# Performance work log

Measured on AMD Instinct MI355X. Metric: run time of the kernel, lower is better.

The kernel has to match this reference:

```python
import jax, jax.numpy as jnp
import numpy as np

EMB = 1024
HEADS = 16
HEAD_SZ = EMB // HEADS
EPS = 1e-5


def _layernorm(x, g, b):
    mu = jnp.mean(x, axis=-1, keepdims=True)
    var = jnp.mean(jnp.square(x - mu), axis=-1, keepdims=True)
    return (x - mu) * jax.lax.rsqrt(var + EPS) * g + b


def setup_inputs() -> dict:
    key = jax.random.key(0)
    ks = jax.random.split(key, 12)
    s_in = 1.0 / np.sqrt(EMB)
    s_h = 1.0 / np.sqrt(4 * EMB)
    return {
        "x": jax.random.normal(ks[0], (4, 1024, EMB), jnp.float32),
        # per-head Q/K/V projections stacked: [H, EMB, HEAD_SZ], no bias
        "wq": jax.random.normal(ks[1], (HEADS, EMB, HEAD_SZ), jnp.float32) * s_in,
        "wk": jax.random.normal(ks[2], (HEADS, EMB, HEAD_SZ), jnp.float32) * s_in,
        "wv": jax.random.normal(ks[3], (HEADS, EMB, HEAD_SZ), jnp.float32) * s_in,
        "w_proj": jax.random.normal(ks[4], (EMB, EMB), jnp.float32) * s_in,
        "b_proj": jnp.zeros((EMB,), jnp.float32),
        "w1": jax.random.normal(ks[5], (EMB, 4 * EMB), jnp.float32) * s_in,
        "b1": jnp.zeros((4 * EMB,), jnp.float32),
        "w2": jax.random.normal(ks[6], (4 * EMB, EMB), jnp.float32) * s_h,
        "b2": jnp.zeros((EMB,), jnp.float32),
        "g1": jnp.ones((EMB,), jnp.float32),
        "be1": jnp.zeros((EMB,), jnp.float32),
        "g2": jnp.ones((EMB,), jnp.float32),
        "be2": jnp.zeros((EMB,), jnp.float32),
    }


def reference(x, wq, wk, wv, w_proj, b_proj, w1, b1, w2, b2, g1, be1, g2, be2):
    B, T, C = x.shape
    # --- self-attention (pre-norm) ---
    h = _layernorm(x, g1, be1)
    q = jnp.einsum("btc,hcd->bhtd", h, wq)
    k = jnp.einsum("btc,hcd->bhtd", h, wk)
    v = jnp.einsum("btc,hcd->bhtd", h, wv)
    scale = 1.0 / jnp.sqrt(jnp.asarray(HEAD_SZ, x.dtype))
    scores = jnp.einsum("bhtd,bhsd->bhts", q, k) * scale  # non-causal: SDPA called with no mask
    attn = jax.nn.softmax(scores, axis=-1)
    o = jnp.einsum("bhts,bhsd->bhtd", attn, v)
    o = o.transpose(0, 2, 1, 3).reshape(B, T, C)  # concat heads (same order as torch.cat)
    sa_out = o @ w_proj + b_proj
    x = x + sa_out
    # --- feed-forward; note ln2 applied twice, faithful to source ---
    t = _layernorm(x, g2, be2)
    t = _layernorm(t, g2, be2)
    ff = jax.nn.relu(t @ w1 + b1) @ w2 + b2
    return x + ff
```

## Files before the change

### kernel.cpp

```cpp
#include <hip/hip_runtime.h>
#include <hip/hip_bf16.h>
#include <math.h>
#include <stdint.h>

typedef __bf16 bf16_t;
typedef __bf16 bf16x4 __attribute__((ext_vector_type(4)));
typedef __bf16 bf16x8 __attribute__((ext_vector_type(8)));
typedef float floatx4 __attribute__((ext_vector_type(4)));

#define BM 128
#define BK 32

__device__ __forceinline__ size_t ftaddr(int m, int k, int KT) {
    return ((size_t)(m >> 4) * KT + (k >> 5)) * 512
         + (((k >> 3) & 3) * 16 + (m & 15)) * 8 + (k & 7);
}

__device__ __forceinline__ void gload16(const void* g, void* lds) {
    __builtin_amdgcn_global_load_lds(
        (__attribute__((address_space(1))) void*)(uintptr_t)g,
        (__attribute__((address_space(3))) void*)(uintptr_t)lds,
        16, 0, 0);
}

template<int N>
__device__ __forceinline__ void waitvm_barrier() {
    if constexpr (N == 0)       asm volatile("s_waitcnt vmcnt(0)\n\ts_barrier" ::: "memory");
    else if constexpr (N == 3)  asm volatile("s_waitcnt vmcnt(3)\n\ts_barrier" ::: "memory");
    else if constexpr (N == 4)  asm volatile("s_waitcnt vmcnt(4)\n\ts_barrier" ::: "memory");
    else if constexpr (N == 6)  asm volatile("s_waitcnt vmcnt(6)\n\ts_barrier" ::: "memory");
    else if constexpr (N == 8)  asm volatile("s_waitcnt vmcnt(8)\n\ts_barrier" ::: "memory");
    else if constexpr (N == 9)  asm volatile("s_waitcnt vmcnt(9)\n\ts_barrier" ::: "memory");
    else if constexpr (N == 12) asm volatile("s_waitcnt vmcnt(12)\n\ts_barrier" ::: "memory");
    else if constexpr (N == 16) asm volatile("s_waitcnt vmcnt(16)\n\ts_barrier" ::: "memory");
    else static_assert(N == 0, "unsupported vmcnt");
}

__device__ __forceinline__ void waitvm_barrier_rt(int n) {
    switch (n) {
    case 12: asm volatile("s_waitcnt vmcnt(12)\n\ts_barrier" ::: "memory"); break;
    case 9:  asm volatile("s_waitcnt vmcnt(9)\n\ts_barrier"  ::: "memory"); break;
    case 8:  asm volatile("s_waitcnt vmcnt(8)\n\ts_barrier"  ::: "memory"); break;
    case 6:  asm volatile("s_waitcnt vmcnt(6)\n\ts_barrier"  ::: "memory"); break;
    case 4:  asm volatile("s_waitcnt vmcnt(4)\n\ts_barrier"  ::: "memory"); break;
    case 3:  asm volatile("s_waitcnt vmcnt(3)\n\ts_barrier"  ::: "memory"); break;
    default: asm volatile("s_waitcnt vmcnt(0)\n\ts_barrier"  ::: "memory"); break;
    }
}

__global__ void prep_kernel(const float* __restrict__ wq, const float* __restrict__ wk,
                            const float* __restrict__ wv, const float* __restrict__ w_proj,
                            const float* __restrict__ w1, const float* __restrict__ w2,
                            bf16_t* __restrict__ WQKVT, bf16_t* __restrict__ WPROJT,
                            bf16_t* __restrict__ W1T, bf16_t* __restrict__ W2T,
                            const float* __restrict__ x, const float* __restrict__ g1,
                            const float* __restrict__ be1, bf16_t* __restrict__ HB)
{
    __shared__ __align__(16) char psm[33024];
    const int tid = threadIdx.x;
    if (blockIdx.x < 3072) {
        float (*tile)[65] = (float(*)[65])psm;
        const int idx = blockIdx.x;
        const float* in; bf16_t* out; int R, C, rt, ct; long nrow0;
        if (idx < 768) {
            const int z = idx >> 8;
            const int hd = (idx >> 4) & 15;
            rt = idx & 15; ct = 0; R = 1024; C = 64;
            in  = (z == 0 ? wq : z == 1 ? wk : wv) + hd * 65536;
            out = WQKVT; nrow0 = z * 1024 + hd * 64;
        } else if (idx < 1024) {
            const int t = idx - 768; rt = t & 15; ct = t >> 4; R = 1024; C = 1024;
            in = w_proj; out = WPROJT; nrow0 = 0;
        } else if (idx < 2048) {
            const int t = idx - 1024; rt = t & 15; ct = t >> 4; R = 1024; C = 4096;
            in = w1; out = W1T; nrow0 = 0;
        } else {
            const int t = idx - 2048; rt = t & 63; ct = t >> 6; R = 4096; C = 1024;
            in = w2; out = W2T; nrow0 = 0;
        }
        const int r0 = rt * 64, c0 = ct * 64;
        const int tr = tid >> 4;
        const int tc = (tid & 15) * 4;
#pragma unroll
        for (int rr = 0; rr < 4; rr++) {
            const int r = tr + rr * 16;
            const float4 v = *(const float4*)&in[(long)(r0 + r) * C + c0 + tc];
            tile[r][tc + 0] = v.x; tile[r][tc + 1] = v.y;
            tile[r][tc + 2] = v.z; tile[r][tc + 3] = v.w;
        }
        __syncthreads();
        const int KT = R >> 5;
        const int w = tid >> 6, l = tid & 63;
        const int c = l >> 4, rr2 = l & 15;
#pragma unroll
        for (int it = 0; it < 2; ++it) {
            const int t8 = it * 4 + w;
            const int kt = t8 >> 2;
            const int nb = t8 & 3;
            const long n = nrow0 + c0 + nb * 16 + rr2;
            const int k = r0 + kt * 32 + c * 8;
            bf16x8 o;
#pragma unroll
            for (int e = 0; e < 8; e++)
                o[e] = (bf16_t)tile[kt * 32 + c * 8 + e][nb * 16 + rr2];
            *(bf16x8*)&out[ftaddr((int)n, k, KT)] = o;
        }
    } else {
        bf16_t (*ybuf)[1032] = (bf16_t(*)[1032])psm;
        const int wave = tid >> 6, lane = tid & 63;
        const int rb = blockIdx.x - 3072;
        float4 gvv[4], bvv[4];
#pragma unroll
        for (int j = 0; j < 4; j++) {
            gvv[j] = ((const float4*)g1)[lane + j * 64];
            bvv[j] = ((const float4*)be1)[lane + j * 64];
        }
#pragma unroll
        for (int rr = 0; rr < 4; ++rr) {
            const int lrow = wave * 4 + rr;
            const float* xr = x + (size_t)(rb * 16 + lrow) * 1024;
            float4 v[4];
            float s = 0.f, s2 = 0.f;
#pragma unroll
            for (int j = 0; j < 4; j++) {
                v[j] = ((const float4*)xr)[lane + j * 64];
                s  += v[j].x + v[j].y + v[j].z + v[j].w;
                s2 += v[j].x * v[j].x + v[j].y * v[j].y + v[j].z * v[j].z + v[j].w * v[j].w;
            }
#pragma unroll
            for (int off = 32; off >= 1; off >>= 1) {
                s  += __shfl_xor(s, off);
                s2 += __shfl_xor(s2, off);
            }
            const float mu = s * (1.0f / 1024.0f);
            const float rs = rsqrtf(fmaxf(s2 * (1.0f / 1024.0f) - mu * mu, 0.f) + 1e-5f);
#pragma unroll
            for (int j = 0; j < 4; j++) {
                bf16x4 o;
                o[0] = (bf16_t)((v[j].x - mu) * rs * gvv[j].x + bvv[j].x);
                o[1] = (bf16_t)((v[j].y - mu) * rs * gvv[j].y + bvv[j].y);
                o[2] = (bf16_t)((v[j].z - mu) * rs * gvv[j].z + bvv[j].z);
                o[3] = (bf16_t)((v[j].w - mu) * rs * gvv[j].w + bvv[j].w);
                *(bf16x4*)&ybuf[lrow][(lane + j * 64) * 4] = o;
            }
        }
        __syncthreads();
        bf16_t* outBase = HB + (size_t)rb * 32 * 512;
#pragma unroll
        for (int it = 0; it < 8; ++it) {
            const int s = it * 256 + tid;
            const int kt = s >> 6, c = (s >> 4) & 3, rr2 = s & 15;
            const bf16x8 val = *(const bf16x8*)&ybuf[rr2][kt * 32 + c * 8];
            *(bf16x8*)&outBase[(size_t)s * 8] = val;
        }
    }
}

__global__ void ln2x_kernel(const float* __restrict__ x, const float* __restrict__ g,
                            const float* __restrict__ b, bf16_t* __restrict__ outb)
{
    __shared__ __align__(16) bf16_t ybuf[16][1032];
    const int tid = threadIdx.x, wave = tid >> 6, lane = tid & 63;
    const int rb = blockIdx.x;
    float4 gvv[4], bvv[4];
#pragma unroll
    for (int j = 0; j < 4; j++) {
        gvv[j] = ((const float4*)g)[lane + j * 64];
        bvv[j] = ((const float4*)b)[lane + j * 64];
    }
#pragma unroll
    for (int rr = 0; rr < 4; ++rr) {
        const int lrow = wave * 4 + rr;
        const float* xr = x + (size_t)(rb * 16 + lrow) * 1024;
        float4 v[4];
        float s = 0.f, s2 = 0.f;
#pragma unroll
        for (int j = 0; j < 4; j++) {
            v[j] = ((const float4*)xr)[lane + j * 64];
            s  += v[j].x + v[j].y + v[j].z + v[j].w;
            s2 += v[j].x * v[j].x + v[j].y * v[j].y + v[j].z * v[j].z + v[j].w * v[j].w;
        }
#pragma unroll
        for (int off = 32; off >= 1; off >>= 1) {
            s  += __shfl_xor(s, off);
            s2 += __shfl_xor(s2, off);
        }
        float mu = s * (1.0f / 1024.0f);
        float rs = rsqrtf(fmaxf(s2 * (1.0f / 1024.0f) - mu * mu, 0.f) + 1e-5f);
        s = 0.f; s2 = 0.f;
#pragma unroll
        for (int j = 0; j < 4; j++) {
            v[j].x = (v[j].x - mu) * rs * gvv[j].x + bvv[j].x;
            v[j].y = (v[j].y - mu) * rs * gvv[j].y + bvv[j].y;
            v[j].z = (v[j].z - mu) * rs * gvv[j].z + bvv[j].z;
            v[j].w = (v[j].w - mu) * rs * gvv[j].w + bvv[j].w;
            s  += v[j].x + v[j].y + v[j].z + v[j].w;
            s2 += v[j].x * v[j].x + v[j].y * v[j].y + v[j].z * v[j].z + v[j].w * v[j].w;
        }
#pragma unroll
        for (int off = 32; off >= 1; off >>= 1) {
            s  += __shfl_xor(s, off);
            s2 += __shfl_xor(s2, off);
        }
        mu = s * (1.0f / 1024.0f);
        rs = rsqrtf(fmaxf(s2 * (1.0f / 1024.0f) - mu * mu, 0.f) + 1e-5f);
#pragma unroll
        for (int j = 0; j < 4; j++) {
            bf16x4 o;
            o[0] = (bf16_t)((v[j].x - mu) * rs * gvv[j].x + bvv[j].x);
            o[1] = (bf16_t)((v[j].y - mu) * rs * gvv[j].y + bvv[j].y);
            o[2] = (bf16_t)((v[j].z - mu) * rs * gvv[j].z + bvv[j].z);
            o[3] = (bf16_t)((v[j].w - mu) * rs * gvv[j].w + bvv[j].w);
            *(bf16x4*)&ybuf[lrow][(lane + j * 64) * 4] = o;
        }
    }
    __syncthreads();
    bf16_t* outBase = outb + (size_t)rb * 32 * 512;
#pragma unroll
    for (int it = 0; it < 8; ++it) {
        const int s = it * 256 + tid;
        const int kt = s >> 6, c = (s >> 4) & 3, rr2 = s & 15;
        const bf16x8 val = *(const bf16x8*)&ybuf[rr2][kt * 32 + c * 8];
        *(bf16x8*)&outBase[(size_t)s * 8] = val;
    }
}

template<int EPI, int BNt, int DEPTH>
__global__ __launch_bounds__(256, 2)
void gemm_bt(const bf16_t* __restrict__ A, const bf16_t* __restrict__ Bt,
             const int K,
             const float* __restrict__ bias, const float* __restrict__ resid,
             float* __restrict__ outf, bf16_t* __restrict__ outb,
             bf16_t* __restrict__ aux1, bf16_t* __restrict__ aux2,
             const int Nout)
{
    constexpr int NFRAG = BNt / 16;
    constexpr int LPS = (BNt == 128) ? 4 : 3;
    constexpr int ASZ = DEPTH * 8 * 512;
    constexpr int BSZ = DEPTH * NFRAG * 512;
    __shared__ __align__(16) bf16_t smem[ASZ + BSZ];
    bf16_t* Asb = smem;
    bf16_t* Bsb = smem + ASZ;
    const int tid  = threadIdx.x;
    const int wave = tid >> 6, lane = tid & 63;
    const int bm = blockIdx.x * BM, bn = blockIdx.y * BNt;
    const int KT = K >> 5;

    floatx4 acc[2][NFRAG];
#pragma unroll
    for (int i = 0; i < 2; i++)
#pragma unroll
        for (int j = 0; j < NFRAG; j++) acc[i][j] = (floatx4){0.f, 0.f, 0.f, 0.f};

    const bf16_t* gA0 = A + ((size_t)(bm / 16 + wave * 2 + 0) * KT) * 512 + lane * 8;
    const bf16_t* gA1 = A + ((size_t)(bm / 16 + wave * 2 + 1) * KT) * 512 + lane * 8;
    const int lA0 = (wave * 2 + 0) * 512;
    const int lA1 = (wave * 2 + 1) * 512;

    const bf16_t* gB0;
    const bf16_t* gB1 = nullptr;
    int lB0, lB1 = 0;
    if (BNt == 128) {
        gB0 = Bt + ((size_t)(bn / 16 + wave * 2 + 0) * KT) * 512 + lane * 8;
        gB1 = Bt + ((size_t)(bn / 16 + wave * 2 + 1) * KT) * 512 + lane * 8;
        lB0 = (wave * 2 + 0) * 512;
        lB1 = (wave * 2 + 1) * 512;
    } else {
        gB0 = Bt + ((size_t)(bn / 16 + wave) * KT) * 512 + lane * 8;
        lB0 = wave * 512;
    }

    auto stage = [&](int t, int bu) {
        const size_t off = (size_t)t * 512;
        gload16(gA0 + off, Asb + bu * 4096 + lA0);
        gload16(gA1 + off, Asb + bu * 4096 + lA1);
        gload16(gB0 + off, Bsb + bu * (NFRAG * 512) + lB0);
        if (BNt == 128) gload16(gB1 + off, Bsb + bu * (NFRAG * 512) + lB1);
    };

    auto compute = [&](int bu) {
        bf16x8 af[2], bfv[NFRAG];
#pragma unroll
        for (int i = 0; i < 2; i++)
            af[i] = *(const bf16x8*)&Asb[bu * 4096 + (wave * 2 + i) * 512 + lane * 8];
#pragma unroll
        for (int j = 0; j < NFRAG; j++)
            bfv[j] = *(const bf16x8*)&Bsb[bu * (NFRAG * 512) + j * 512 + lane * 8];
#pragma unroll
        for (int i = 0; i < 2; i++)
#pragma unroll
            for (int j = 0; j < NFRAG; j++)
                acc[i][j] = __builtin_amdgcn_mfma_f32_16x16x32_bf16(af[i], bfv[j], acc[i][j], 0, 0, 0);
    };

    const int NT = K / BK;
#pragma unroll
    for (int i = 0; i < DEPTH - 1; ++i) stage(i, i);
    int bu = 0;
    for (int t = 0; t <= NT - DEPTH; ++t) {
        waitvm_barrier<LPS * (DEPTH - 2)>();
        stage(t + DEPTH - 1, bu == 0 ? DEPTH - 1 : bu - 1);
        compute(bu);
        bu = (bu + 1 == DEPTH) ? 0 : bu + 1;
    }
#pragma unroll
    for (int j = DEPTH - 2; j >= 0; --j) {
        waitvm_barrier_rt(LPS * j);
        compute(bu);
        bu = (bu + 1 == DEPTH) ? 0 : bu + 1;
    }

    const int er = (lane >> 4) * 4, ec = lane & 15;
    if (EPI == 0 && bn >= 2048) {
        __syncthreads();
        bf16_t* scr = smem;
#pragma unroll
        for (int i = 0; i < 2; i++)
#pragma unroll
            for (int j = 0; j < NFRAG; j++)
#pragma unroll
                for (int r = 0; r < 4; r++)
                    scr[(j * 16 + ec) * 136 + wave * 32 + i * 16 + er + r] =
                        (bf16_t)acc[i][j][r];
        __syncthreads();
        const int bq = bm >> 10, tmod = bm & 1023, h0 = (bn - 2048) >> 6;
#pragma unroll
        for (int it = 0; it < 8; ++it) {
            const int c = it * 256 + tid;
            const int dl = c >> 4, t16 = c & 15;
            const bf16x8 val = *(const bf16x8*)&scr[dl * 136 + t16 * 8];
            const int h = h0 + (dl >> 6), dd = dl & 63;
            *(bf16x8*)&aux2[(size_t)((bq * 16 + h) * 64 + dd) * 1024 + tmod + t16 * 8] = val;
        }
        return;
    }
#pragma unroll
    for (int i = 0; i < 2; i++) {
#pragma unroll
        for (int j = 0; j < NFRAG; j++) {
            const int col = bn + j * 16 + ec;
#pragma unroll
            for (int r = 0; r < 4; r++) {
                const int row = bm + wave * 32 + i * 16 + er + r;
                const float v = acc[i][j][r];
                if (EPI == 0) {
                    const int b = row >> 10, t = row & 1023;
                    if (col < 1024) {
                        const int h = col >> 6, d = col & 63;
                        outb[(size_t)((b * 16 + h) * 1024 + t) * 64 + d] = (bf16_t)v;
                    } else {
                        const int c2 = col - 1024, h = c2 >> 6, d = c2 & 63;
                        aux1[(size_t)((b * 16 + h) * 1024 + t) * 64 + d] = (bf16_t)v;
                    }
                } else if (EPI == 1 || EPI == 3) {
                    const size_t idx = (size_t)row * Nout + col;
                    outf[idx] = v + bias[col] + resid[idx];
                } else if (EPI == 2) {
                    outb[ftaddr(row, col, Nout >> 5)] = (bf16_t)fmaxf(v + bias[col], 0.f);
                }
            }
        }
    }
}

__global__ __launch_bounds__(256, 4)
void attn_kernel(const bf16_t* __restrict__ Q, const bf16_t* __restrict__ Kg,
                 const bf16_t* __restrict__ Vt, bf16_t* __restrict__ Og)
{
    __shared__ __align__(16) bf16_t Ks[2][4096];
    __shared__ __align__(16) bf16_t Vs[2][4096];
    __shared__ __align__(16) bf16_t Ps[4][1024];
    const int tid = threadIdx.x, wave = tid >> 6, lane = tid & 63;
    const int bh = blockIdx.y;
    const int b = bh >> 4, h = bh & 15;
    const int q0 = blockIdx.x * 64 + wave * 16;
    const bf16_t* Qb = Q + (size_t)bh * 65536;
    const char* Kb = (const char*)(Kg + (size_t)bh * 65536);
    const char* Vb = (const char*)(Vt + (size_t)bh * 65536);
    const int fr = lane & 15, g = lane >> 4, fk = g * 8;

    const bf16x8 qf0 = *(const bf16x8*)&Qb[(size_t)(q0 + fr) * 64 + fk];
    const bf16x8 qf1 = *(const bf16x8*)&Qb[(size_t)(q0 + fr) * 64 + 32 + fk];

    floatx4 o[4];
#pragma unroll
    for (int dt = 0; dt < 4; dt++) o[dt] = (floatx4){0.f, 0.f, 0.f, 0.f};
    float lsum[4] = {0.f, 0.f, 0.f, 0.f};
    bf16_t* pw = &Ps[wave][0];
    const float sscale = 0.125f * 1.44269504088896f;

    auto stage = [&](int s0, int bu) {
#pragma unroll
        for (int t = 0; t < 2; t++) {
            const int j = wave * 2 + t;
            gload16(Kb + (size_t)(s0 + lane) * 128 + j * 16, &Ks[bu][j * 512]);
            gload16(Vb + (size_t)lane * 2048 + (size_t)s0 * 2 + j * 16, &Vs[bu][j * 512]);
        }
    };

    stage(0, 0);
    int bu = 0;
    for (int it = 0; it < 16; ++it) {
        __syncthreads();
        if (it < 15) stage((it + 1) * 64, bu ^ 1);
        const bf16_t* Kl = Ks[bu];
        const bf16_t* Vl = Vs[bu];

        floatx4 sacc[4];
#pragma unroll
        for (int ss = 0; ss < 4; ss++) sacc[ss] = (floatx4){0.f, 0.f, 0.f, 0.f};
#pragma unroll
        for (int c = 0; c < 2; c++) {
            const int ch = c * 4 + g;
            const bf16x8 qf = (c == 0) ? qf0 : qf1;
#pragma unroll
            for (int ss = 0; ss < 4; ss++) {
                const bf16x8 kf = *(const bf16x8*)&Kl[ch * 512 + (ss * 16 + fr) * 8];
                sacc[ss] = __builtin_amdgcn_mfma_f32_16x16x32_bf16(qf, kf, sacc[ss], 0, 0, 0);
            }
        }
#pragma unroll
        for (int ss = 0; ss < 4; ss++) {
#pragma unroll
            for (int r = 0; r < 4; r++) {
                const float p = __builtin_amdgcn_exp2f(sacc[ss][r] * sscale);
                lsum[r] += p;
                const int q = g * 4 + r;
                pw[(ss * 2 + (fr >> 3)) * 128 + q * 8 + (fr & 7)] = (bf16_t)p;
            }
        }
        asm volatile("s_waitcnt lgkmcnt(0)" ::: "memory");
#pragma unroll
        for (int c = 0; c < 2; c++) {
            const int ch = c * 4 + g;
            const bf16x8 pf = *(const bf16x8*)&pw[ch * 128 + fr * 8];
#pragma unroll
            for (int dt = 0; dt < 4; dt++) {
                const bf16x8 vf = *(const bf16x8*)&Vl[ch * 512 + (dt * 16 + fr) * 8];
                o[dt] = __builtin_amdgcn_mfma_f32_16x16x32_bf16(pf, vf, o[dt], 0, 0, 0);
            }
        }
        asm volatile("" ::: "memory");
        bu ^= 1;
    }
#pragma unroll
    for (int r = 0; r < 4; r++) {
        float l = lsum[r];
        l += __shfl_xor(l, 1);
        l += __shfl_xor(l, 2);
        l += __shfl_xor(l, 4);
        l += __shfl_xor(l, 8);
        lsum[r] = 1.0f / l;
    }
    const int tq = q0 + g * 4;
#pragma unroll
    for (int dt = 0; dt < 4; dt++) {
#pragma unroll
        for (int r = 0; r < 4; r++) {
            const int m = b * 1024 + tq + r;
            const int k = h * 64 + dt * 16 + fr;
            Og[ftaddr(m, k, 32)] = (bf16_t)(o[dt][r] * lsum[r]);
        }
    }
}

extern "C" void kernel_launch(void* const* d_in, const int* in_sizes, int n_in,
                              void* d_out, int out_size, void* d_ws, size_t ws_size,
                              hipStream_t stream)
{
    const float* x      = (const float*)d_in[0];
    const float* wq     = (const float*)d_in[1];
    const float* wk     = (const float*)d_in[2];
    const float* wv     = (const float*)d_in[3];
    const float* w_proj = (const float*)d_in[4];
    const float* b_proj = (const float*)d_in[5];
    const float* w1     = (const float*)d_in[6];
    const float* b1     = (const float*)d_in[7];
    const float* w2     = (const float*)d_in[8];
    const float* b2     = (const float*)d_in[9];
    const float* g1     = (const float*)d_in[10];
    const float* be1    = (const float*)d_in[11];
    const float* g2     = (const float*)d_in[12];
    const float* be2    = (const float*)d_in[13];
    float* out = (float*)d_out;
    char* ws = (char*)d_ws;

    bf16_t* WQKVT = (bf16_t*)(ws + 0x0000000);
    bf16_t* WPROJT= (bf16_t*)(ws + 0x0600000);
    bf16_t* W1T   = (bf16_t*)(ws + 0x0800000);
    bf16_t* W2T   = (bf16_t*)(ws + 0x1000000);
    bf16_t* HB    = (bf16_t*)(ws + 0x1800000);
    bf16_t* Qb    = (bf16_t*)(ws + 0x2000000);
    bf16_t* Kb    = (bf16_t*)(ws + 0x2800000);
    bf16_t* Vtb   = (bf16_t*)(ws + 0x3000000);
    bf16_t* AO    = (bf16_t*)(ws + 0x3800000);
    float*  X2    = (float*)(ws + 0x4000000);
    bf16_t* TB    = (bf16_t*)(ws + 0x2800000);
    bf16_t* FF1B  = (bf16_t*)(ws + 0x5000000);

    dim3 blk(256);
    prep_kernel<<<3328, blk, 0, stream>>>(wq, wk, wv, w_proj, w1, w2,
                                          WQKVT, WPROJT, W1T, W2T,
                                          x, g1, be1, HB);
    gemm_bt<0, 128, 4><<<dim3(32, 24), blk, 0, stream>>>(HB, WQKVT, 1024, nullptr, nullptr,
                                                         nullptr, Qb, Kb, Vtb, 3072);
    attn_kernel<<<dim3(16, 64), blk, 0, stream>>>(Qb, Kb, Vtb, AO);
    gemm_bt<1, 64, 6><<<dim3(32, 16), blk, 0, stream>>>(AO, WPROJT, 1024, b_proj, x,
                                                        X2, nullptr, nullptr, nullptr, 1024);
    ln2x_kernel<<<256, blk, 0, stream>>>(X2, g2, be2, TB);
    gemm_bt<2, 128, 4><<<dim3(32, 32), blk, 0, stream>>>(TB, W1T, 1024, b1, nullptr,
                                                         nullptr, FF1B, nullptr, nullptr, 4096);
    gemm_bt<3, 64, 6><<<dim3(32, 16), blk, 0, stream>>>(FF1B, W2T, 4096, b2, X2,
                                                        out, nullptr, nullptr, nullptr, 1024);
}
```

Measured before the change: 300.6 us.

## Remap attention blocks per XCD, interleave softmax with PV MFMAs, retune GEMM depths

The attention kernel now remaps block indices so that all query tiles of a batch-head pair land on the same XCD, which should improve L2 reuse of K/V. Its inner loop is reordered so that half the softmax exponentials are written before the first PV MFMA group, giving staggered overlap, and s_setprio raises wave priority around MFMA bursts. The GEMMs get retuned pipeline depths (5 for the BN=128 variants, 4 for BN=64) and the BN=64 variant targets 3 blocks per CU via launch bounds. These changes trade shared-memory depth for occupancy, and the register cap could cause spills.

```diff
diff --git a/kernel.cpp b/kernel.cpp
--- a/kernel.cpp
+++ b/kernel.cpp
@@ -226,7 +226,7 @@
 }
 
 template<int EPI, int BNt, int DEPTH>
-__global__ __launch_bounds__(256, 2)
+__global__ __launch_bounds__(256, (BNt == 64 ? 3 : 2))
 void gemm_bt(const bf16_t* __restrict__ A, const bf16_t* __restrict__ Bt,
              const int K,
              const float* __restrict__ bias, const float* __restrict__ resid,
@@ -371,9 +371,12 @@
     __shared__ __align__(16) bf16_t Vs[2][4096];
     __shared__ __align__(16) bf16_t Ps[4][1024];
     const int tid = threadIdx.x, wave = tid >> 6, lane = tid & 63;
-    const int bh = blockIdx.y;
+    const int lin = blockIdx.x + (blockIdx.y << 4);
+    const int xcd = lin & 7, idx = lin >> 3;
+    const int bh = xcd * 8 + (idx >> 4);
+    const int qt = idx & 15;
     const int b = bh >> 4, h = bh & 15;
-    const int q0 = blockIdx.x * 64 + wave * 16;
+    const int q0 = qt * 64 + wave * 16;
     const bf16_t* Qb = Q + (size_t)bh * 65536;
     const char* Kb = (const char*)(Kg + (size_t)bh * 65536);
     const char* Vb = (const char*)(Vt + (size_t)bh * 65536);
@@ -409,18 +412,20 @@
         floatx4 sacc[4];
 #pragma unroll
         for (int ss = 0; ss < 4; ss++) sacc[ss] = (floatx4){0.f, 0.f, 0.f, 0.f};
-#pragma unroll
-        for (int c = 0; c < 2; c++) {
-            const int ch = c * 4 + g;
-            const bf16x8 qf = (c == 0) ? qf0 : qf1;
-#pragma unroll
-            for (int ss = 0; ss < 4; ss++) {
+        __builtin_amdgcn_s_setprio(1);
+#pragma unroll
+        for (int ss = 0; ss < 4; ss++) {
+#pragma unroll
+            for (int c = 0; c < 2; c++) {
+                const int ch = c * 4 + g;
+                const bf16x8 qf = (c == 0) ? qf0 : qf1;
                 const bf16x8 kf = *(const bf16x8*)&Kl[ch * 512 + (ss * 16 + fr) * 8];
                 sacc[ss] = __builtin_amdgcn_mfma_f32_16x16x32_bf16(qf, kf, sacc[ss], 0, 0, 0);
             }
         }
-#pragma unroll
-        for (int ss = 0; ss < 4; ss++) {
+        __builtin_amdgcn_s_setprio(0);
+#pragma unroll
+        for (int ss = 0; ss < 2; ss++) {
 #pragma unroll
             for (int r = 0; r < 4; r++) {
                 const float p = __builtin_amdgcn_exp2f(sacc[ss][r] * sscale);
@@ -431,14 +436,37 @@
         }
         asm volatile("s_waitcnt lgkmcnt(0)" ::: "memory");
 #pragma unroll
-        for (int c = 0; c < 2; c++) {
-            const int ch = c * 4 + g;
+        for (int ss = 2; ss < 4; ss++) {
+#pragma unroll
+            for (int r = 0; r < 4; r++) {
+                const float p = __builtin_amdgcn_exp2f(sacc[ss][r] * sscale);
+                lsum[r] += p;
+                const int q = g * 4 + r;
+                pw[(ss * 2 + (fr >> 3)) * 128 + q * 8 + (fr & 7)] = (bf16_t)p;
+            }
+        }
+        {
+            const int ch = g;
             const bf16x8 pf = *(const bf16x8*)&pw[ch * 128 + fr * 8];
+            __builtin_amdgcn_s_setprio(1);
 #pragma unroll
             for (int dt = 0; dt < 4; dt++) {
                 const bf16x8 vf = *(const bf16x8*)&Vl[ch * 512 + (dt * 16 + fr) * 8];
                 o[dt] = __builtin_amdgcn_mfma_f32_16x16x32_bf16(pf, vf, o[dt], 0, 0, 0);
             }
+            __builtin_amdgcn_s_setprio(0);
+        }
+        asm volatile("s_waitcnt lgkmcnt(0)" ::: "memory");
+        {
+            const int ch = 4 + g;
+            const bf16x8 pf = *(const bf16x8*)&pw[ch * 128 + fr * 8];
+            __builtin_amdgcn_s_setprio(1);
+#pragma unroll
+            for (int dt = 0; dt < 4; dt++) {
+                const bf16x8 vf = *(const bf16x8*)&Vl[ch * 512 + (dt * 16 + fr) * 8];
+                o[dt] = __builtin_amdgcn_mfma_f32_16x16x32_bf16(pf, vf, o[dt], 0, 0, 0);
+            }
+            __builtin_amdgcn_s_setprio(0);
         }
         asm volatile("" ::: "memory");
         bu ^= 1;
@@ -502,14 +530,14 @@
     prep_kernel<<<3328, blk, 0, stream>>>(wq, wk, wv, w_proj, w1, w2,
                                           WQKVT, WPROJT, W1T, W2T,
                                           x, g1, be1, HB);
-    gemm_bt<0, 128, 4><<<dim3(32, 24), blk, 0, stream>>>(HB, WQKVT, 1024, nullptr, nullptr,
+    gemm_bt<0, 128, 5><<<dim3(32, 24), blk, 0, stream>>>(HB, WQKVT, 1024, nullptr, nullptr,
                                                          nullptr, Qb, Kb, Vtb, 3072);
     attn_kernel<<<dim3(16, 64), blk, 0, stream>>>(Qb, Kb, Vtb, AO);
-    gemm_bt<1, 64, 6><<<dim3(32, 16), blk, 0, stream>>>(AO, WPROJT, 1024, b_proj, x,
+    gemm_bt<1, 64, 4><<<dim3(32, 16), blk, 0, stream>>>(AO, WPROJT, 1024, b_proj, x,
                                                         X2, nullptr, nullptr, nullptr, 1024);
     ln2x_kernel<<<256, blk, 0, stream>>>(X2, g2, be2, TB);
-    gemm_bt<2, 128, 4><<<dim3(32, 32), blk, 0, stream>>>(TB, W1T, 1024, b1, nullptr,
+    gemm_bt<2, 128, 5><<<dim3(32, 32), blk, 0, stream>>>(TB, W1T, 1024, b1, nullptr,
                                                          nullptr, FF1B, nullptr, nullptr, 4096);
-    gemm_bt<3, 64, 6><<<dim3(32, 16), blk, 0, stream>>>(FF1B, W2T, 4096, b2, X2,
+    gemm_bt<3, 64, 4><<<dim3(32, 16), blk, 0, stream>>>(FF1B, W2T, 4096, b2, X2,
                                                         out, nullptr, nullptr, nullptr, 1024);
 }
```

After: 303.9 us. About the same (+1.1%).
